# Performance work log

Hardware: AMD Instinct MI355X
Metric: run time of the kernel (lower is better)

## Reference

```python
import jax, jax.numpy as jnp
import numpy as np

TWO_PI = 2.0 * np.pi
OMEGA = 1.0  # frequency scale from init


def setup_inputs() -> dict:
    key = jax.random.key(0)
    ks = jax.random.split(key, 10)
    B, G, D = 2, 32, 3
    C_IN, C, C_OUT, F, L = 4, 128, 2, 128, 4  # in/model/out channels, freqs, n_spectral_convs
    a = jax.random.normal(ks[0], (B, G, G, G, C_IN), dtype=jnp.float32)
    x = jax.random.uniform(ks[1], (B, G, G, G, D), dtype=jnp.float32)
    y = jax.random.uniform(ks[2], (B, G, G, G, D), dtype=jnp.float32)
    fc_in_w = jax.random.normal(ks[3], (C_IN, C), dtype=jnp.float32) / np.sqrt(C_IN)
    fc_in_b = jnp.zeros((C,), dtype=jnp.float32)
    freqs = jax.random.normal(ks[4], (L, F, D), dtype=jnp.float32)  # per-layer spatial frequencies
    w_real = jax.random.normal(ks[5], (L, C, C, F), dtype=jnp.float32) * 0.05
    w_imag = jax.random.normal(ks[6], (L, C, C, F), dtype=jnp.float32) * 0.05
    fc_out_w = jax.random.normal(ks[7], (C, C_OUT), dtype=jnp.float32) / np.sqrt(C)
    fc_out_b = jnp.zeros((C_OUT,), dtype=jnp.float32)
    return {"a": a, "x": x, "y": y, "fc_in_w": fc_in_w, "fc_in_b": fc_in_b,
            "freqs": freqs, "w_real": w_real, "w_imag": w_imag,
            "fc_out_w": fc_out_w, "fc_out_b": fc_out_b}


def _spectral_conv(hf, xin, xout, k, Wc):
    # hf: (B, N, C) real; xin/xout: (B, N, D); k: (F, D); Wc: (C, C, F) complex
    N = hf.shape[1]
    ang_in = TWO_PI * OMEGA * jnp.einsum('bnd,fd->bnf', xin, k)
    phi_in = jnp.exp(-1j * ang_in.astype(jnp.complex64))          # (B, N, F)
    H = jnp.einsum('bnc,bnf->bcf', hf.astype(jnp.complex64), phi_in) / N  # forward transform
    G = jnp.einsum('bcf,cof->bof', H, Wc)                          # per-frequency channel mixing
    ang_out = TWO_PI * OMEGA * jnp.einsum('bnd,fd->bnf', xout, k)
    phi_out = jnp.exp(1j * ang_out.astype(jnp.complex64))          # (B, N, F)
    return jnp.real(jnp.einsum('bof,bnf->bno', G, phi_out))       # inverse evaluation at xout


def reference(a, x, y, fc_in_w, fc_in_b, freqs, w_real, w_imag, fc_out_w, fc_out_b):
    B = a.shape[0]
    spatial = a.shape[1:4]
    hf = jnp.einsum('...i,io->...o', a, fc_in_w) + fc_in_b
    hf = hf.reshape(B, -1, hf.shape[-1])               # (B, N, C)
    xf = x.reshape(B, -1, x.shape[-1])                 # (B, N, D)
    yf = y.reshape(B, -1, y.shape[-1])
    L = freqs.shape[0]
    for l in range(L):
        Wc = (w_real[l] + 1j * w_imag[l]).astype(jnp.complex64)
        pts_out = xf if l < L - 1 else yf              # last conv queries at y
        hf = jax.nn.gelu(_spectral_conv(hf, xf, pts_out, freqs[l], Wc))
    u = jnp.einsum('bnc,co->bno', hf, fc_out_w) + fc_out_b
    return u.reshape(B, *spatial, fc_out_w.shape[-1])
```

## Files before the change

### kernel.cpp

```cpp
#include <hip/hip_runtime.h>
#include <math.h>

#define Bb 2
#define Nn 32768
#define Cc 128
#define Ff 128
#define LL 4
#define SKN 128
#define PS 16448

typedef __attribute__((ext_vector_type(8))) short short8;
typedef __attribute__((ext_vector_type(4))) float float4v;
typedef __attribute__((ext_vector_type(2))) unsigned int uint2v;
typedef unsigned short ushort_t;
typedef unsigned int uint_t;

union frag_cast { short8 s; uint_t u[4]; };
union vec8 { float4v v[2]; float s[8]; };

__device__ inline uint_t asu(float f) { union { float f; uint_t u; } x; x.f = f; return x.u; }
__device__ inline float asf(uint_t u) { union { uint_t u; float f; } x; x.u = u; return x.f; }
__device__ inline uint_t pack_hi(float v0, float v1) {
    return __builtin_amdgcn_perm(asu(v1), asu(v0), 0x07060302u);
}
__device__ inline float resid(float v) { return v - asf(asu(v) & 0xffff0000u); }

typedef __attribute__((address_space(1))) const uint_t guint;
typedef __attribute__((address_space(3))) uint_t luint;
__device__ inline void gload16(const uint_t* g, uint_t* l) {
    __builtin_amdgcn_global_load_lds((guint*)g, (luint*)l, 16, 0, 0);
}

#define LBAR() asm volatile("s_waitcnt lgkmcnt(0)\n\ts_barrier" ::: "memory")

__global__ __launch_bounds__(256) void prep_xt(const float* __restrict__ x,
                                               const float* __restrict__ y,
                                               float* __restrict__ xT,
                                               float* __restrict__ yT) {
    int i = blockIdx.x * 256 + threadIdx.x;
    int b = i >> 15, n = i & 32767;
    const float* xp = x + (size_t)i * 3;
    const float* yp = y + (size_t)i * 3;
    size_t base = ((size_t)(b * 3) << 15) + n;
    xT[base] = xp[0]; xT[base + (1 << 15)] = xp[1]; xT[base + (2 << 15)] = xp[2];
    yT[base] = yp[0]; yT[base + (1 << 15)] = yp[1]; yT[base + (2 << 15)] = yp[2];
}

__global__ __launch_bounds__(256) void in_proj(const float* __restrict__ a,
                                               const float* __restrict__ w,
                                               const float* __restrict__ bias,
                                               uint_t* __restrict__ hfTh,
                                               uint_t* __restrict__ hfTl) {
    int idx = blockIdx.x * 256 + threadIdx.x;
    int np = idx & 16383;
    int c = (idx >> 14) & 127;
    int b = idx >> 21;
    int n = np * 2;
    const float* ap = a + (((size_t)(b << 15)) + n) * 4;
    float s0 = bias[c], s1 = s0;
#pragma unroll
    for (int i = 0; i < 4; ++i) { s0 += ap[i] * w[i * Cc + c]; s1 += ap[4 + i] * w[i * Cc + c]; }
    hfTh[idx] = pack_hi(s0, s1);
    hfTl[idx] = pack_hi(resid(s0), resid(s1));
}

__global__ __launch_bounds__(512, 2) void fwd_lds(const uint_t* __restrict__ hfTh,
                                                  const uint_t* __restrict__ hfTl,
                                                  const float* __restrict__ xT,
                                                  const float* __restrict__ freqs,
                                                  float* __restrict__ Spart) {
    __shared__ __align__(16) uint_t Ah_s[2][2048], Al_s[2][2048];

    const int sk = blockIdx.x;
    const int b = blockIdx.y;
    const int tid = threadIdx.x, lane = tid & 63, wave = tid >> 6;
    const int h = wave & 1, wn = wave >> 1;
    const int fr = lane & 15, kg = lane >> 4;

    float kx[2], ky[2], kz[2];
#pragma unroll
    for (int ni = 0; ni < 2; ++ni) {
        int f = wn * 32 + ni * 16 + fr;
        kx[ni] = freqs[f * 3 + 0];
        ky[ni] = freqs[f * 3 + 1];
        kz[ni] = freqs[f * 3 + 2];
    }

    const float* xb = xT + ((size_t)(b * 3) << 15);

    const int srow = wave * 16 + (lane >> 2);
    const size_t gbase = ((size_t)(b * 128 + srow) << 14) + (size_t)((lane & 3) * 4);
    const int npair0 = sk * 128;

    float4v acc[8][2];
#pragma unroll
    for (int mi = 0; mi < 8; ++mi)
#pragma unroll
        for (int ni = 0; ni < 2; ++ni) acc[mi][ni] = (float4v){0.f, 0.f, 0.f, 0.f};

    vec8 X0[2], X1[2], X2[2];
    gload16(hfTh + gbase + npair0, &Ah_s[0][wave * 256]);
    gload16(hfTl + gbase + npair0, &Al_s[0][wave * 256]);
    {
        const int nbase = sk * 256 + kg * 8;
        X0[0].v[0] = *(const float4v*)(xb + nbase);
        X0[0].v[1] = *(const float4v*)(xb + nbase + 4);
        X1[0].v[0] = *(const float4v*)(xb + (1 << 15) + nbase);
        X1[0].v[1] = *(const float4v*)(xb + (1 << 15) + nbase + 4);
        X2[0].v[0] = *(const float4v*)(xb + (2 << 15) + nbase);
        X2[0].v[1] = *(const float4v*)(xb + (2 << 15) + nbase + 4);
    }

#pragma unroll
    for (int kt = 0; kt < 8; ++kt) {
        const int cur = kt & 1, nxt = cur ^ 1;
        __syncthreads();
        if (kt < 7) {
            gload16(hfTh + gbase + npair0 + (kt + 1) * 16, &Ah_s[nxt][wave * 256]);
            gload16(hfTl + gbase + npair0 + (kt + 1) * 16, &Al_s[nxt][wave * 256]);
            const int nbase2 = sk * 256 + (kt + 1) * 32 + kg * 8;
            X0[nxt].v[0] = *(const float4v*)(xb + nbase2);
            X0[nxt].v[1] = *(const float4v*)(xb + nbase2 + 4);
            X1[nxt].v[0] = *(const float4v*)(xb + (1 << 15) + nbase2);
            X1[nxt].v[1] = *(const float4v*)(xb + (1 << 15) + nbase2 + 4);
            X2[nxt].v[0] = *(const float4v*)(xb + (2 << 15) + nbase2);
            X2[nxt].v[1] = *(const float4v*)(xb + (2 << 15) + nbase2 + 4);
        }
        float r[16], tv[16];
#pragma unroll
        for (int ni = 0; ni < 2; ++ni)
#pragma unroll
            for (int q = 0; q < 4; ++q) {
                float rv0 = X0[cur].s[2 * q] * kx[ni] + X1[cur].s[2 * q] * ky[ni] + X2[cur].s[2 * q] * kz[ni];
                float rv1 = X0[cur].s[2 * q + 1] * kx[ni] + X1[cur].s[2 * q + 1] * ky[ni] + X2[cur].s[2 * q + 1] * kz[ni];
                r[ni * 8 + 2 * q] = __builtin_amdgcn_fractf(rv0);
                r[ni * 8 + 2 * q + 1] = __builtin_amdgcn_fractf(rv1);
            }
        if (h) {
#pragma unroll
            for (int i = 0; i < 16; ++i) tv[i] = __builtin_amdgcn_sinf(r[i]);
        } else {
#pragma unroll
            for (int i = 0; i < 16; ++i) tv[i] = __builtin_amdgcn_cosf(r[i]);
        }
        frag_cast bhf[2], blf[2];
#pragma unroll
        for (int ni = 0; ni < 2; ++ni)
#pragma unroll
            for (int q = 0; q < 4; ++q) {
                float v0 = tv[ni * 8 + 2 * q], v1 = tv[ni * 8 + 2 * q + 1];
                bhf[ni].u[q] = pack_hi(v0, v1);
                blf[ni].u[q] = pack_hi(resid(v0), resid(v1));
            }
#pragma unroll
        for (int mi = 0; mi < 8; ++mi) {
            frag_cast ah, al;
            ah.s = *(const short8*)&Ah_s[cur][(mi * 16 + fr) * 16 + kg * 4];
            al.s = *(const short8*)&Al_s[cur][(mi * 16 + fr) * 16 + kg * 4];
#pragma unroll
            for (int ni = 0; ni < 2; ++ni) {
                acc[mi][ni] = __builtin_amdgcn_mfma_f32_16x16x32_bf16(ah.s, bhf[ni].s, acc[mi][ni], 0, 0, 0);
                acc[mi][ni] = __builtin_amdgcn_mfma_f32_16x16x32_bf16(ah.s, blf[ni].s, acc[mi][ni], 0, 0, 0);
                acc[mi][ni] = __builtin_amdgcn_mfma_f32_16x16x32_bf16(al.s, bhf[ni].s, acc[mi][ni], 0, 0, 0);
            }
        }
    }

    float* op = Spart + (size_t)((b * 2 + h) * SKN + sk) * PS;
#pragma unroll
    for (int mi = 0; mi < 8; ++mi)
#pragma unroll
        for (int ni = 0; ni < 2; ++ni)
#pragma unroll
            for (int r2 = 0; r2 < 4; ++r2) {
                int c = mi * 16 + kg * 4 + r2;
                int f = wn * 32 + ni * 16 + fr;
                op[c * 128 + f] = acc[mi][ni][r2];
            }
}

__global__ __launch_bounds__(256) void reduce_kernel(const float* __restrict__ Spart,
                                                     float* __restrict__ S) {
    __shared__ float red[4][64];
    const int chunk = blockIdx.x, bh = blockIdx.y;
    const int tid = threadIdx.x;
    const int cfl = tid & 63, q = tid >> 6;
    const float* p = Spart + (size_t)bh * SKN * PS + (size_t)(q * 32) * PS + chunk * 64 + cfl;
    float s = 0.0f;
#pragma unroll 8
    for (int k = 0; k < 32; ++k) s += p[(size_t)k * PS];
    red[q][cfl] = s;
    __syncthreads();
    if (tid < 64) {
        float t = red[0][tid] + red[1][tid] + red[2][tid] + red[3][tid];
        S[bh * 16384 + chunk * 64 + tid] = t;
    }
}

__global__ __launch_bounds__(256) void mix_kernel(const float* __restrict__ S,
                                                  const float* __restrict__ Wre,
                                                  const float* __restrict__ Wim,
                                                  uint_t* __restrict__ Gh,
                                                  uint_t* __restrict__ Gl) {
    __shared__ float Stile[4][128][16];
    const int ot = blockIdx.x;
    const int ft = blockIdx.y;
    const int tid = threadIdx.x;
    const int fl = tid & 15, ol = (tid >> 4) & 1, cg = tid >> 5;
    const int o = ot * 2 + ol, f0 = ft * 16;

    for (int i = tid; i < 8192; i += 256) {
        int bh = i >> 11, c = (i >> 4) & 127, ff = i & 15;
        Stile[bh][c][ff] = S[(size_t)bh * 16384 + c * 128 + f0 + ff];
    }
    __syncthreads();

    float g0 = 0.f, g1 = 0.f, g2 = 0.f, g3 = 0.f;
#pragma unroll 4
    for (int c = cg * 16; c < cg * 16 + 16; ++c) {
        float wr = Wre[((size_t)(c * 128 + o)) * 128 + f0 + fl];
        float wi = Wim[((size_t)(c * 128 + o)) * 128 + f0 + fl];
        float sc0 = Stile[0][c][fl], ss0 = Stile[1][c][fl];
        float sc1 = Stile[2][c][fl], ss1 = Stile[3][c][fl];
        g0 += sc0 * wr + ss0 * wi;  g1 += ss0 * wr - sc0 * wi;
        g2 += sc1 * wr + ss1 * wi;  g3 += ss1 * wr - sc1 * wi;
    }
    __syncthreads();
    float4v* rp = (float4v*)Stile;
    rp[cg * 32 + ol * 16 + fl] = (float4v){g0, g1, g2, g3};
    __syncthreads();
    if (tid < 32) {
        int tol = tid >> 4, tfl = tid & 15;
        float4v r = rp[tid];
#pragma unroll
        for (int j = 1; j < 8; ++j) r += rp[j * 32 + tid];
        const float invN = 1.0f / (float)Nn;
        float gre0 = r[0] * invN, gmi0 = r[1] * invN;
        float gre1 = r[2] * invN, gmi1 = r[3] * invN;
        int oo = ot * 2 + tol;
        Gh[(0 * 128 + oo) * 128 + f0 + tfl] = pack_hi(gre0, gmi0);
        Gl[(0 * 128 + oo) * 128 + f0 + tfl] = pack_hi(resid(gre0), resid(gmi0));
        Gh[(1 * 128 + oo) * 128 + f0 + tfl] = pack_hi(gre1, gmi1);
        Gl[(1 * 128 + oo) * 128 + f0 + tfl] = pack_hi(resid(gre1), resid(gmi1));
    }
}

template <int LAST>
__global__ __launch_bounds__(256, 2) void inv_reg(const uint_t* __restrict__ Gh,
                                                  const uint_t* __restrict__ Gl,
                                                  const float* __restrict__ ptsT,
                                                  const float* __restrict__ freqs,
                                                  uint_t* __restrict__ hfTh,
                                                  uint_t* __restrict__ hfTl,
                                                  const float* __restrict__ ow,
                                                  const float* __restrict__ ob,
                                                  float* __restrict__ u) {
    __shared__ __align__(16) float kxs[128], kys[128], kzs[128];
    __shared__ __align__(16) uint_t Ah_s[4096];
    __shared__ __align__(16) uint_t Al_s[4096];
    __shared__ float redo[4][32][2];
    const int nt = blockIdx.x, b = blockIdx.y;
    const int tid = threadIdx.x, lane = tid & 63, wn = tid >> 6;
    const int fr = lane & 15, kg = lane >> 4;

    if (tid < 128) {
        kxs[tid] = freqs[tid * 3 + 0];
        kys[tid] = freqs[tid * 3 + 1];
        kzs[tid] = freqs[tid * 3 + 2];
    }

    frag_cast bh[8][2], bl[8][2];
#pragma unroll
    for (int kt = 0; kt < 8; ++kt)
#pragma unroll
        for (int ni = 0; ni < 2; ++ni) {
            size_t gi = ((size_t)(b * 128 + wn * 32 + ni * 16 + fr)) * 128 + kt * 16 + kg * 4;
            bh[kt][ni].s = *(const short8*)(Gh + gi);
            bl[kt][ni].s = *(const short8*)(Gl + gi);
        }

    float w0v[2], w1v[2];
    if (LAST) {
#pragma unroll
        for (int ni = 0; ni < 2; ++ni) {
            int o = wn * 32 + ni * 16 + fr;
            w0v[ni] = ow[o * 2 + 0];
            w1v[ni] = ow[o * 2 + 1];
        }
    }

    const float* pb = ptsT + ((size_t)(b * 3) << 15);
    const int stripe0 = nt * 64;

    float px[2][2], py[2][2], pz[2][2];
#pragma unroll
    for (int it = 0; it < 2; ++it)
#pragma unroll
        for (int mi = 0; mi < 2; ++mi) {
            int n = stripe0 + it * 32 + mi * 16 + fr;
            px[it][mi] = pb[n]; py[it][mi] = pb[(1 << 15) + n]; pz[it][mi] = pb[(2 << 15) + n];
        }

    __syncthreads();

#pragma unroll
    for (int it = 0; it < 2; ++it) {
        const int n0 = stripe0 + it * 32;

#pragma unroll
        for (int kk = 0; kk < 2; ++kk) {
            const int kt = wn * 2 + kk;
            float4v kxv = *(const float4v*)&kxs[kt * 16 + kg * 4];
            float4v kyv = *(const float4v*)&kys[kt * 16 + kg * 4];
            float4v kzv = *(const float4v*)&kzs[kt * 16 + kg * 4];
#pragma unroll
            for (int mi = 0; mi < 2; ++mi) {
                frag_cast ah, al;
#pragma unroll
                for (int q = 0; q < 4; ++q) {
                    float rev = px[it][mi] * kxv[q] + py[it][mi] * kyv[q] + pz[it][mi] * kzv[q];
                    float rr = __builtin_amdgcn_fractf(rev);
                    float cv = __builtin_amdgcn_cosf(rr);
                    float sv = __builtin_amdgcn_sinf(rr);
                    ah.u[q] = pack_hi(cv, sv);
                    al.u[q] = pack_hi(resid(cv), resid(sv));
                }
                *(short8*)&Ah_s[((mi * 8 + kt) * 64 + lane) * 4] = ah.s;
                *(short8*)&Al_s[((mi * 8 + kt) * 64 + lane) * 4] = al.s;
            }
        }
        LBAR();

        float4v acc[2][2];
#pragma unroll
        for (int mi = 0; mi < 2; ++mi)
#pragma unroll
            for (int ni = 0; ni < 2; ++ni) acc[mi][ni] = (float4v){0.f, 0.f, 0.f, 0.f};

#pragma unroll
        for (int kt = 0; kt < 8; ++kt) {
#pragma unroll
            for (int mi = 0; mi < 2; ++mi) {
                frag_cast ah, al;
                ah.s = *(const short8*)&Ah_s[((mi * 8 + kt) * 64 + lane) * 4];
                al.s = *(const short8*)&Al_s[((mi * 8 + kt) * 64 + lane) * 4];
#pragma unroll
                for (int ni = 0; ni < 2; ++ni) {
                    acc[mi][ni] = __builtin_amdgcn_mfma_f32_16x16x32_bf16(ah.s, bh[kt][ni].s, acc[mi][ni], 0, 0, 0);
                    acc[mi][ni] = __builtin_amdgcn_mfma_f32_16x16x32_bf16(ah.s, bl[kt][ni].s, acc[mi][ni], 0, 0, 0);
                    acc[mi][ni] = __builtin_amdgcn_mfma_f32_16x16x32_bf16(al.s, bh[kt][ni].s, acc[mi][ni], 0, 0, 0);
                }
            }
        }
        LBAR();

        float ps[2][2][4];
        if (LAST) {
#pragma unroll
            for (int mi = 0; mi < 2; ++mi)
#pragma unroll
                for (int j = 0; j < 2; ++j)
#pragma unroll
                    for (int r2 = 0; r2 < 4; ++r2) ps[mi][j][r2] = 0.f;
        }
#pragma unroll
        for (int mi = 0; mi < 2; ++mi)
#pragma unroll
            for (int ni = 0; ni < 2; ++ni) {
                float g[4];
#pragma unroll
                for (int r2 = 0; r2 < 4; ++r2) {
                    float v = acc[mi][ni][r2];
                    float u2 = 1.5957691216057308f * (v + 0.044715f * v * v * v);
                    float t = 1.0f - 2.0f / (1.0f + __expf(u2));
                    g[r2] = 0.5f * v * (1.0f + t);
                }
                if (!LAST) {
                    int o = wn * 32 + ni * 16 + fr;
                    int nb = n0 + mi * 16 + kg * 4;
                    size_t di = ((size_t)(b * 128 + o) << 14) + (nb >> 1);
                    uint2v hv = { pack_hi(g[0], g[1]), pack_hi(g[2], g[3]) };
                    uint2v lv = { pack_hi(resid(g[0]), resid(g[1])), pack_hi(resid(g[2]), resid(g[3])) };
                    *(uint2v*)(hfTh + di) = hv;
                    *(uint2v*)(hfTl + di) = lv;
                } else {
#pragma unroll
                    for (int r2 = 0; r2 < 4; ++r2) {
                        ps[mi][0][r2] += g[r2] * w0v[ni];
                        ps[mi][1][r2] += g[r2] * w1v[ni];
                    }
                }
            }

        if (LAST) {
#pragma unroll
            for (int mi = 0; mi < 2; ++mi)
#pragma unroll
                for (int j = 0; j < 2; ++j)
#pragma unroll
                    for (int r2 = 0; r2 < 4; ++r2) {
                        float v = ps[mi][j][r2];
                        v += __shfl_xor(v, 1);
                        v += __shfl_xor(v, 2);
                        v += __shfl_xor(v, 4);
                        v += __shfl_xor(v, 8);
                        ps[mi][j][r2] = v;
                    }
            if (fr == 0) {
#pragma unroll
                for (int mi = 0; mi < 2; ++mi)
#pragma unroll
                    for (int r2 = 0; r2 < 4; ++r2) {
                        redo[wn][mi * 16 + kg * 4 + r2][0] = ps[mi][0][r2];
                        redo[wn][mi * 16 + kg * 4 + r2][1] = ps[mi][1][r2];
                    }
            }
            LBAR();
            if (tid < 64) {
                int nl = tid >> 1, j = tid & 1;
                float val = ob[j] + redo[0][nl][j] + redo[1][nl][j] + redo[2][nl][j] + redo[3][nl][j];
                u[((size_t)((b << 15) + n0 + nl)) * 2 + j] = val;
            }
        }
    }
}

extern "C" void kernel_launch(void* const* d_in, const int* in_sizes, int n_in,
                              void* d_out, int out_size, void* d_ws, size_t ws_size,
                              hipStream_t stream) {
    const float* a        = (const float*)d_in[0];
    const float* x        = (const float*)d_in[1];
    const float* y        = (const float*)d_in[2];
    const float* fc_in_w  = (const float*)d_in[3];
    const float* fc_in_b  = (const float*)d_in[4];
    const float* freqs    = (const float*)d_in[5];
    const float* w_real   = (const float*)d_in[6];
    const float* w_imag   = (const float*)d_in[7];
    const float* fc_out_w = (const float*)d_in[8];
    const float* fc_out_b = (const float*)d_in[9];
    float* out = (float*)d_out;

    uint_t* ws    = (uint_t*)d_ws;
    uint_t* hfTh  = ws;
    uint_t* hfTl  = hfTh + (size_t)Bb * Cc * Nn / 2;
    float*  Spart = (float*)(hfTl + (size_t)Bb * Cc * Nn / 2);
    float*  S     = Spart + (size_t)Bb * 2 * SKN * PS;
    uint_t* Gh    = (uint_t*)(S + (size_t)Bb * 2 * Cc * Ff);
    uint_t* Gl    = Gh + (size_t)Bb * Cc * Ff;
    float*  xT    = (float*)(Gl + (size_t)Bb * Cc * Ff);
    float*  yT    = xT + (size_t)Bb * 3 * Nn;

    prep_xt<<<(Bb * Nn) / 256, 256, 0, stream>>>(x, y, xT, yT);
    in_proj<<<(Bb * Cc * Nn / 2) / 256, 256, 0, stream>>>(a, fc_in_w, fc_in_b, hfTh, hfTl);

    for (int l = 0; l < LL; ++l) {
        const float* k   = freqs  + (size_t)l * Ff * 3;
        const float* Wre = w_real + (size_t)l * Cc * Cc * Ff;
        const float* Wim = w_imag + (size_t)l * Cc * Cc * Ff;
        const float* pT  = (l < LL - 1) ? xT : yT;

        fwd_lds<<<dim3(SKN, Bb), 512, 0, stream>>>(hfTh, hfTl, xT, k, Spart);
        reduce_kernel<<<dim3(256, 4), 256, 0, stream>>>(Spart, S);
        mix_kernel<<<dim3(64, 8), 256, 0, stream>>>(S, Wre, Wim, Gh, Gl);
        if (l < LL - 1) {
            inv_reg<0><<<dim3(512, Bb), 256, 0, stream>>>(Gh, Gl, pT, k, hfTh, hfTl,
                                                          nullptr, nullptr, nullptr);
        } else {
            inv_reg<1><<<dim3(512, Bb), 256, 0, stream>>>(Gh, Gl, pT, k, hfTh, hfTl,
                                                          fc_out_w, fc_out_b, out);
        }
    }
}
```

Baseline: 367.5 us.

## Split inverse kernel across eight waves with one output tile per wave

The inverse evaluation kernel now runs 512 threads per block instead of 256. Each of the eight waves owns a 16-channel output slice instead of 32, so it keeps half as many G fragments in registers. Each wave also computes the phase factors for a single k-tile per phase. The aim is lower register pressure and higher occupancy, at the cost of more barriers, a wider reduction in the last layer, and less MFMA work per wave to hide latency.

```diff
diff --git a/kernel.cpp b/kernel.cpp
--- a/kernel.cpp
+++ b/kernel.cpp
@@ -246,7 +246,7 @@
 }
 
 template <int LAST>
-__global__ __launch_bounds__(256, 2) void inv_reg(const uint_t* __restrict__ Gh,
+__global__ __launch_bounds__(512, 4) void inv_reg(const uint_t* __restrict__ Gh,
                                                   const uint_t* __restrict__ Gl,
                                                   const float* __restrict__ ptsT,
                                                   const float* __restrict__ freqs,
@@ -258,7 +258,7 @@
     __shared__ __align__(16) float kxs[128], kys[128], kzs[128];
     __shared__ __align__(16) uint_t Ah_s[4096];
     __shared__ __align__(16) uint_t Al_s[4096];
-    __shared__ float redo[4][32][2];
+    __shared__ float redo[8][32][2];
     const int nt = blockIdx.x, b = blockIdx.y;
     const int tid = threadIdx.x, lane = tid & 63, wn = tid >> 6;
     const int fr = lane & 15, kg = lane >> 4;
@@ -269,87 +269,73 @@
         kzs[tid] = freqs[tid * 3 + 2];
     }
 
-    frag_cast bh[8][2], bl[8][2];
-#pragma unroll
-    for (int kt = 0; kt < 8; ++kt)
-#pragma unroll
-        for (int ni = 0; ni < 2; ++ni) {
-            size_t gi = ((size_t)(b * 128 + wn * 32 + ni * 16 + fr)) * 128 + kt * 16 + kg * 4;
-            bh[kt][ni].s = *(const short8*)(Gh + gi);
-            bl[kt][ni].s = *(const short8*)(Gl + gi);
-        }
-
-    float w0v[2], w1v[2];
+    frag_cast bh[8], bl[8];
+#pragma unroll
+    for (int kt = 0; kt < 8; ++kt) {
+        size_t gi = ((size_t)(b * 128 + wn * 16 + fr)) * 128 + kt * 16 + kg * 4;
+        bh[kt].s = *(const short8*)(Gh + gi);
+        bl[kt].s = *(const short8*)(Gl + gi);
+    }
+
+    float w0v = 0.f, w1v = 0.f;
     if (LAST) {
-#pragma unroll
-        for (int ni = 0; ni < 2; ++ni) {
-            int o = wn * 32 + ni * 16 + fr;
-            w0v[ni] = ow[o * 2 + 0];
-            w1v[ni] = ow[o * 2 + 1];
-        }
+        int o = wn * 16 + fr;
+        w0v = ow[o * 2 + 0];
+        w1v = ow[o * 2 + 1];
     }
 
     const float* pb = ptsT + ((size_t)(b * 3) << 15);
-    const int stripe0 = nt * 64;
-
-    float px[2][2], py[2][2], pz[2][2];
-#pragma unroll
-    for (int it = 0; it < 2; ++it)
-#pragma unroll
-        for (int mi = 0; mi < 2; ++mi) {
-            int n = stripe0 + it * 32 + mi * 16 + fr;
-            px[it][mi] = pb[n]; py[it][mi] = pb[(1 << 15) + n]; pz[it][mi] = pb[(2 << 15) + n];
-        }
+    const int n0 = nt * 64;
+
+    float px[4], py[4], pz[4];
+#pragma unroll
+    for (int m = 0; m < 4; ++m) {
+        int n = n0 + m * 16 + fr;
+        px[m] = pb[n]; py[m] = pb[(1 << 15) + n]; pz[m] = pb[(2 << 15) + n];
+    }
 
     __syncthreads();
 
 #pragma unroll
-    for (int it = 0; it < 2; ++it) {
-        const int n0 = stripe0 + it * 32;
-
-#pragma unroll
-        for (int kk = 0; kk < 2; ++kk) {
-            const int kt = wn * 2 + kk;
+    for (int ph = 0; ph < 2; ++ph) {
+        {
+            const int kt = wn;
             float4v kxv = *(const float4v*)&kxs[kt * 16 + kg * 4];
             float4v kyv = *(const float4v*)&kys[kt * 16 + kg * 4];
             float4v kzv = *(const float4v*)&kzs[kt * 16 + kg * 4];
 #pragma unroll
-            for (int mi = 0; mi < 2; ++mi) {
+            for (int mi2 = 0; mi2 < 2; ++mi2) {
+                const int m = ph * 2 + mi2;
                 frag_cast ah, al;
 #pragma unroll
                 for (int q = 0; q < 4; ++q) {
-                    float rev = px[it][mi] * kxv[q] + py[it][mi] * kyv[q] + pz[it][mi] * kzv[q];
+                    float rev = px[m] * kxv[q] + py[m] * kyv[q] + pz[m] * kzv[q];
                     float rr = __builtin_amdgcn_fractf(rev);
                     float cv = __builtin_amdgcn_cosf(rr);
                     float sv = __builtin_amdgcn_sinf(rr);
                     ah.u[q] = pack_hi(cv, sv);
                     al.u[q] = pack_hi(resid(cv), resid(sv));
                 }
-                *(short8*)&Ah_s[((mi * 8 + kt) * 64 + lane) * 4] = ah.s;
-                *(short8*)&Al_s[((mi * 8 + kt) * 64 + lane) * 4] = al.s;
+                *(short8*)&Ah_s[((mi2 * 8 + kt) * 64 + lane) * 4] = ah.s;
+                *(short8*)&Al_s[((mi2 * 8 + kt) * 64 + lane) * 4] = al.s;
             }
         }
         LBAR();
 
-        float4v acc[2][2];
-#pragma unroll
-        for (int mi = 0; mi < 2; ++mi)
-#pragma unroll
-            for (int ni = 0; ni < 2; ++ni) acc[mi][ni] = (float4v){0.f, 0.f, 0.f, 0.f};
+        float4v acc[2];
+#pragma unroll
+        for (int mi2 = 0; mi2 < 2; ++mi2) acc[mi2] = (float4v){0.f, 0.f, 0.f, 0.f};
 
 #pragma unroll
         for (int kt = 0; kt < 8; ++kt) {
 #pragma unroll
-            for (int mi = 0; mi < 2; ++mi) {
+            for (int mi2 = 0; mi2 < 2; ++mi2) {
                 frag_cast ah, al;
-                ah.s = *(const short8*)&Ah_s[((mi * 8 + kt) * 64 + lane) * 4];
-                al.s = *(const short8*)&Al_s[((mi * 8 + kt) * 64 + lane) * 4];
-#pragma unroll
-                for (int ni = 0; ni < 2; ++ni) {
-                    acc[mi][ni] = __builtin_amdgcn_mfma_f32_16x16x32_bf16(ah.s, bh[kt][ni].s, acc[mi][ni], 0, 0, 0);
-                    acc[mi][ni] = __builtin_amdgcn_mfma_f32_16x16x32_bf16(ah.s, bl[kt][ni].s, acc[mi][ni], 0, 0, 0);
-                    acc[mi][ni] = __builtin_amdgcn_mfma_f32_16x16x32_bf16(al.s, bh[kt][ni].s, acc[mi][ni], 0, 0, 0);
-                }
+                ah.s = *(const short8*)&Ah_s[((mi2 * 8 + kt) * 64 + lane) * 4];
+                al.s = *(const short8*)&Al_s[((mi2 * 8 + kt) * 64 + lane) * 4];
+                acc[mi2] = __builtin_amdgcn_mfma_f32_16x16x32_bf16(ah.s, bh[kt].s, acc[mi2], 0, 0, 0);
+                acc[mi2] = __builtin_amdgcn_mfma_f32_16x16x32_bf16(ah.s, bl[kt].s, acc[mi2], 0, 0, 0);
+                acc[mi2] = __builtin_amdgcn_mfma_f32_16x16x32_bf16(al.s, bh[kt].s, acc[mi2], 0, 0, 0);
             }
         }
         LBAR();
@@ -357,70 +343,72 @@
         float ps[2][2][4];
         if (LAST) {
 #pragma unroll
-            for (int mi = 0; mi < 2; ++mi)
+            for (int mi2 = 0; mi2 < 2; ++mi2)
 #pragma unroll
                 for (int j = 0; j < 2; ++j)
 #pragma unroll
-                    for (int r2 = 0; r2 < 4; ++r2) ps[mi][j][r2] = 0.f;
-        }
-#pragma unroll
-        for (int mi = 0; mi < 2; ++mi)
-#pragma unroll
-            for (int ni = 0; ni < 2; ++ni) {
-                float g[4];
+                    for (int r2 = 0; r2 < 4; ++r2) ps[mi2][j][r2] = 0.f;
+        }
+#pragma unroll
+        for (int mi2 = 0; mi2 < 2; ++mi2) {
+            const int m = ph * 2 + mi2;
+            float g[4];
+#pragma unroll
+            for (int r2 = 0; r2 < 4; ++r2) {
+                float v = acc[mi2][r2];
+                float u2 = 1.5957691216057308f * (v + 0.044715f * v * v * v);
+                float t = 1.0f - 2.0f / (1.0f + __expf(u2));
+                g[r2] = 0.5f * v * (1.0f + t);
+            }
+            if (!LAST) {
+                int o = wn * 16 + fr;
+                int nb = n0 + m * 16 + kg * 4;
+                size_t di = ((size_t)(b * 128 + o) << 14) + (nb >> 1);
+                uint2v hv = { pack_hi(g[0], g[1]), pack_hi(g[2], g[3]) };
+                uint2v lv = { pack_hi(resid(g[0]), resid(g[1])), pack_hi(resid(g[2]), resid(g[3])) };
+                *(uint2v*)(hfTh + di) = hv;
+                *(uint2v*)(hfTl + di) = lv;
+            } else {
 #pragma unroll
                 for (int r2 = 0; r2 < 4; ++r2) {
-                    float v = acc[mi][ni][r2];
-                    float u2 = 1.5957691216057308f * (v + 0.044715f * v * v * v);
-                    float t = 1.0f - 2.0f / (1.0f + __expf(u2));
-                    g[r2] = 0.5f * v * (1.0f + t);
+                    ps[mi2][0][r2] += g[r2] * w0v;
+                    ps[mi2][1][r2] += g[r2] * w1v;
                 }
-                if (!LAST) {
-                    int o = wn * 32 + ni * 16 + fr;
-                    int nb = n0 + mi * 16 + kg * 4;
-                    size_t di = ((size_t)(b * 128 + o) << 14) + (nb >> 1);
-                    uint2v hv = { pack_hi(g[0], g[1]), pack_hi(g[2], g[3]) };
-                    uint2v lv = { pack_hi(resid(g[0]), resid(g[1])), pack_hi(resid(g[2]), resid(g[3])) };
-                    *(uint2v*)(hfTh + di) = hv;
-                    *(uint2v*)(hfTl + di) = lv;
-                } else {
+            }
+        }
+
+        if (LAST) {
+#pragma unroll
+            for (int mi2 = 0; mi2 < 2; ++mi2)
+#pragma unroll
+                for (int j = 0; j < 2; ++j)
 #pragma unroll
                     for (int r2 = 0; r2 < 4; ++r2) {
-                        ps[mi][0][r2] += g[r2] * w0v[ni];
-                        ps[mi][1][r2] += g[r2] * w1v[ni];
-                    }
-                }
-            }
-
-        if (LAST) {
-#pragma unroll
-            for (int mi = 0; mi < 2; ++mi)
-#pragma unroll
-                for (int j = 0; j < 2; ++j)
-#pragma unroll
-                    for (int r2 = 0; r2 < 4; ++r2) {
-                        float v = ps[mi][j][r2];
+                        float v = ps[mi2][j][r2];
                         v += __shfl_xor(v, 1);
                         v += __shfl_xor(v, 2);
                         v += __shfl_xor(v, 4);
                         v += __shfl_xor(v, 8);
-                        ps[mi][j][r2] = v;
+                        ps[mi2][j][r2] = v;
                     }
             if (fr == 0) {
 #pragma unroll
-                for (int mi = 0; mi < 2; ++mi)
+                for (int mi2 = 0; mi2 < 2; ++mi2)
 #pragma unroll
                     for (int r2 = 0; r2 < 4; ++r2) {
-                        redo[wn][mi * 16 + kg * 4 + r2][0] = ps[mi][0][r2];
-                        redo[wn][mi * 16 + kg * 4 + r2][1] = ps[mi][1][r2];
+                        redo[wn][mi2 * 16 + kg * 4 + r2][0] = ps[mi2][0][r2];
+                        redo[wn][mi2 * 16 + kg * 4 + r2][1] = ps[mi2][1][r2];
                     }
             }
             LBAR();
             if (tid < 64) {
                 int nl = tid >> 1, j = tid & 1;
-                float val = ob[j] + redo[0][nl][j] + redo[1][nl][j] + redo[2][nl][j] + redo[3][nl][j];
-                u[((size_t)((b << 15) + n0 + nl)) * 2 + j] = val;
-            }
+                float val = ob[j];
+#pragma unroll
+                for (int w8 = 0; w8 < 8; ++w8) val += redo[w8][nl][j];
+                u[((size_t)((b << 15) + n0 + ph * 32 + nl)) * 2 + j] = val;
+            }
+            LBAR();
         }
     }
 }
@@ -463,10 +451,10 @@
         reduce_kernel<<<dim3(256, 4), 256, 0, stream>>>(Spart, S);
         mix_kernel<<<dim3(64, 8), 256, 0, stream>>>(S, Wre, Wim, Gh, Gl);
         if (l < LL - 1) {
-            inv_reg<0><<<dim3(512, Bb), 256, 0, stream>>>(Gh, Gl, pT, k, hfTh, hfTl,
+            inv_reg<0><<<dim3(512, Bb), 512, 0, stream>>>(Gh, Gl, pT, k, hfTh, hfTl,
                                                           nullptr, nullptr, nullptr);
         } else {
-            inv_reg<1><<<dim3(512, Bb), 256, 0, stream>>>(Gh, Gl, pT, k, hfTh, hfTl,
+            inv_reg<1><<<dim3(512, Bb), 512, 0, stream>>>(Gh, Gl, pT, k, hfTh, hfTl,
                                                           fc_out_w, fc_out_b, out);
         }
     }
```

After: 368.5 us. Within noise of the previous version (+0.3%).
